# Optimization experiments

Hardware: AMD Instinct MI355X
Metric: run time of the kernel (lower is better)

The kernel has to match this reference:

```python
import jax, jax.numpy as jnp
import numpy as np

N, E, D, G, L = 100000, 1600000, 32, 64, 3
BN_EPS = 1e-5


def setup_inputs() -> dict:
    key = jax.random.key(0)
    ks = jax.random.split(key, 8)
    x = jax.random.normal(ks[0], (N, D), dtype=jnp.float32)
    edge_index = jax.random.randint(ks[1], (2, E), 0, N, dtype=jnp.int64)
    batch = jnp.sort(jax.random.randint(ks[2], (N,), 0, G, dtype=jnp.int64))
    layer_weights = jnp.ones((L,), dtype=jnp.float32)
    # linears[i]: Linear(D->D) + BN(D) (inference-mode stats) ; L of them
    lin_W = jax.random.normal(ks[3], (L, D, D), dtype=jnp.float32) * (1.0 / np.sqrt(D))
    lin_b = jnp.zeros((L, D), dtype=jnp.float32)
    lin_gamma = jnp.ones((L, D), dtype=jnp.float32)
    lin_beta = jnp.zeros((L, D), dtype=jnp.float32)
    lin_mean = jnp.zeros((L, D), dtype=jnp.float32)
    lin_var = jnp.ones((L, D), dtype=jnp.float32)
    # GINConv MLPs: Linear(D->D) + BN(D) + ELU ; L-1 of them
    conv_W = jax.random.normal(ks[4], (L - 1, D, D), dtype=jnp.float32) * (1.0 / np.sqrt(D))
    conv_b = jnp.zeros((L - 1, D), dtype=jnp.float32)
    conv_gamma = jnp.ones((L - 1, D), dtype=jnp.float32)
    conv_beta = jnp.zeros((L - 1, D), dtype=jnp.float32)
    conv_mean = jnp.zeros((L - 1, D), dtype=jnp.float32)
    conv_var = jnp.ones((L - 1, D), dtype=jnp.float32)
    return {"x": x, "edge_index": edge_index, "batch": batch,
            "layer_weights": layer_weights,
            "lin_W": lin_W, "lin_b": lin_b, "lin_gamma": lin_gamma,
            "lin_beta": lin_beta, "lin_mean": lin_mean, "lin_var": lin_var,
            "conv_W": conv_W, "conv_b": conv_b, "conv_gamma": conv_gamma,
            "conv_beta": conv_beta, "conv_mean": conv_mean, "conv_var": conv_var}


def _mlp(h, W, b, gamma, beta, mean, var):
    # Linear -> BatchNorm1d (inference stats) -> ELU
    h = h @ W + b
    h = (h - mean) * (gamma * jax.lax.rsqrt(var + BN_EPS)) + beta
    return jax.nn.elu(h)


def reference(x, edge_index, batch, layer_weights,
              lin_W, lin_b, lin_gamma, lin_beta, lin_mean, lin_var,
              conv_W, conv_b, conv_gamma, conv_beta, conv_mean, conv_var):
    src, dst = edge_index[0], edge_index[1]
    z = _mlp(x, lin_W[0], lin_b[0], lin_gamma[0], lin_beta[0], lin_mean[0], lin_var[0])
    Z = layer_weights[0] * z
    out = jax.ops.segment_max(z, batch, num_segments=G)  # global_max_pool
    for l in range(1, L):
        # GINConv (eps=0): x' = MLP(x + sum_{j->i} x_j)
        agg = jax.ops.segment_sum(x[src], dst, num_segments=N)
        x = _mlp(x + agg, conv_W[l - 1], conv_b[l - 1], conv_gamma[l - 1],
                 conv_beta[l - 1], conv_mean[l - 1], conv_var[l - 1])
        z = layer_weights[l] * _mlp(x, lin_W[l], lin_b[l], lin_gamma[l],
                                    lin_beta[l], lin_mean[l], lin_var[l])
        Z = Z + z
        out = out + jax.ops.segment_max(z, batch, num_segments=G)
    # dropout p=0.0 is identity
    return (out, Z, x)
```

## Files before the change

kernel.cpp:

```cpp
#include <hip/hip_runtime.h>
#include <math.h>

#define N_NODES 100000
#define N_EDGES 1600000
#define DIM 32
#define N_GROUPS 64
#define BN_EPS 1e-5f

#define BIN_NODES 128
#define NBINS ((N_NODES + BIN_NODES - 1) / BIN_NODES)
#define EPB_HIST 2048
#define HIST_BLOCKS ((N_EDGES + EPB_HIST - 1) / EPB_HIST)
#define EPB_SCAT 8192
#define SCAT_SUB (EPB_SCAT / EPB_HIST)
#define SCAT_BLOCKS ((N_EDGES + EPB_SCAT - 1) / EPB_SCAT)
#define GF2_BLOCKS ((N_NODES + 127) / 128)
#define CNT_PAD 16

#define CS_BPG 16
#define CS_BLOCKS ((NBINS + CS_BPG - 1) / CS_BPG)

#define HLS 40

typedef __attribute__((ext_vector_type(8))) short short8;
typedef __attribute__((ext_vector_type(4))) float f32x4;
typedef __attribute__((ext_vector_type(4))) unsigned u32x4;

__device__ __forceinline__ unsigned enc_f32(float f) {
    unsigned u = __float_as_uint(f);
    return (u & 0x80000000u) ? ~u : (u | 0x80000000u);
}
__device__ __forceinline__ float dec_f32(unsigned u) {
    return (u & 0x80000000u) ? __uint_as_float(u & 0x7FFFFFFFu) : __uint_as_float(~u);
}
__device__ __forceinline__ unsigned short f2bf(float f) {
    unsigned u = __float_as_uint(f);
    u += 0x7FFFu + ((u >> 16) & 1u);
    return (unsigned short)(u >> 16);
}

__global__ __launch_bounds__(256) void foldhist_kernel(
        const float* __restrict__ lin_W, const float* __restrict__ lin_b,
        const float* __restrict__ lin_gamma, const float* __restrict__ lin_beta,
        const float* __restrict__ lin_mean, const float* __restrict__ lin_var,
        const float* __restrict__ conv_W, const float* __restrict__ conv_b,
        const float* __restrict__ conv_gamma, const float* __restrict__ conv_beta,
        const float* __restrict__ conv_mean, const float* __restrict__ conv_var,
        float* __restrict__ shf, unsigned short* __restrict__ Wfb,
        unsigned short* __restrict__ x0b, unsigned short* __restrict__ xbufb,
        const int* __restrict__ dst, int* __restrict__ blockcnt)
{
    __shared__ int cnt[NBINS];
    int bid = blockIdx.x;
    int t = threadIdx.x;
    if (bid >= 6) {
        int hb = bid - 6;
        for (int b = t; b < NBINS; b += 256) cnt[b] = 0;
        __syncthreads();
        int base = hb * EPB_HIST;
        for (int i = 0; i < EPB_HIST / 256; ++i) {
            int e = base + i * 256 + t;
            if (e < N_EDGES) atomicAdd(&cnt[dst[e] >> 7], 1);
        }
        __syncthreads();
        for (int b = t; b < NBINS; b += 256)
            blockcnt[(size_t)hb * NBINS + b] = cnt[b];
        return;
    }
    if (bid == 5) {
        if (t < DIM) {
            x0b[(size_t)N_NODES * DIM + t] = 0;
            xbufb[(size_t)N_NODES * DIM + t] = 0;
        }
        return;
    }
    const float *W, *b, *gm, *bt, *mn, *vr;
    if (bid < 3) {
        W = lin_W + bid * DIM * DIM; b = lin_b + bid * DIM; gm = lin_gamma + bid * DIM;
        bt = lin_beta + bid * DIM;   mn = lin_mean + bid * DIM; vr = lin_var + bid * DIM;
    } else {
        int c = bid - 3;
        W = conv_W + c * DIM * DIM; b = conv_b + c * DIM; gm = conv_gamma + c * DIM;
        bt = conv_beta + c * DIM;   mn = conv_mean + c * DIM; vr = conv_var + c * DIM;
    }
    for (int idx = t; idx < DIM * DIM; idx += 256) {
        int j = idx & (DIM - 1);
        float scale = gm[j] / sqrtf(vr[j] + BN_EPS);
        Wfb[bid * DIM * DIM + idx] = f2bf(W[idx] * scale);
    }
    if (t < DIM) {
        float scale = gm[t] / sqrtf(vr[t] + BN_EPS);
        shf[bid * DIM + t] = (b[t] - mn[t]) * scale + bt[t];
    }
}

__global__ __launch_bounds__(256) void colsum_scan_kernel(
        const int* __restrict__ blockcnt,
        int* __restrict__ bincnt,
        int* __restrict__ binoff, int* __restrict__ bincur,
        int* __restrict__ done)
{
    __shared__ int sums[16][CS_BPG];
    __shared__ int sscan[256];
    __shared__ int tick;
    int t = threadIdx.x;
    int g = blockIdx.x;
    int bl = t & 15;
    int h0 = t >> 4;
    int b = g * CS_BPG + bl;
    int s = 0;
    if (b < NBINS) {
        for (int hb = h0; hb < HIST_BLOCKS; hb += 16)
            s += blockcnt[(size_t)hb * NBINS + b];
    }
    sums[h0][bl] = s;
    __syncthreads();
    if (t < CS_BPG && (g * CS_BPG + t) < NBINS) {
        int tot = 0;
#pragma unroll
        for (int h = 0; h < 16; ++h) tot += sums[h][t];
        atomicExch(&bincnt[(g * CS_BPG + t) * CNT_PAD], tot);
    }
    __threadfence();
    __syncthreads();
    if (t == 0) tick = atomicAdd(done, 1);
    __syncthreads();
    if (tick == (int)gridDim.x - 1) {
        int i0 = t * 4;
        int c0 = (i0 + 0 < NBINS) ? atomicAdd(&bincnt[(i0 + 0) * CNT_PAD], 0) : 0;
        int c1 = (i0 + 1 < NBINS) ? atomicAdd(&bincnt[(i0 + 1) * CNT_PAD], 0) : 0;
        int c2 = (i0 + 2 < NBINS) ? atomicAdd(&bincnt[(i0 + 2) * CNT_PAD], 0) : 0;
        int c3 = (i0 + 3 < NBINS) ? atomicAdd(&bincnt[(i0 + 3) * CNT_PAD], 0) : 0;
        int local = c0 + c1 + c2 + c3;
        sscan[t] = local;
        __syncthreads();
        for (int off = 1; off < 256; off <<= 1) {
            int u = (t >= off) ? sscan[t - off] : 0;
            __syncthreads();
            sscan[t] += u;
            __syncthreads();
        }
        int run = sscan[t] - local;
        if (i0 + 0 < NBINS) { binoff[i0 + 0] = run; bincur[(i0 + 0) * CNT_PAD] = run; run += c0; }
        if (i0 + 1 < NBINS) { binoff[i0 + 1] = run; bincur[(i0 + 1) * CNT_PAD] = run; run += c1; }
        if (i0 + 2 < NBINS) { binoff[i0 + 2] = run; bincur[(i0 + 2) * CNT_PAD] = run; run += c2; }
        if (i0 + 3 < NBINS) { binoff[i0 + 3] = run; bincur[(i0 + 3) * CNT_PAD] = run; run += c3; }
        if (t == 0) binoff[NBINS] = N_EDGES;
    }
}

__global__ __launch_bounds__(512) void scatter_linz_kernel(
        const int* __restrict__ src, const int* __restrict__ dst,
        int* __restrict__ bincur, unsigned* __restrict__ binbuf,
        const int* __restrict__ blockcnt,
        const float* __restrict__ x0, unsigned short* __restrict__ x0b,
        const unsigned short* __restrict__ Wb, const float* __restrict__ shfv,
        const int* __restrict__ batch, const float* __restrict__ lw_ptr,
        float* __restrict__ Z, unsigned* __restrict__ segmax)
{
    __shared__ int smem[NBINS];
    int t = threadIdx.x;

    if (blockIdx.x < SCAT_BLOCKS) {
        int* pos = smem;
        for (int b = t; b < NBINS; b += 512) {
            int c = 0;
#pragma unroll
            for (int k = 0; k < SCAT_SUB; ++k) {
                int r = blockIdx.x * SCAT_SUB + k;
                if (r < HIST_BLOCKS)
                    c += blockcnt[(size_t)r * NBINS + b];
            }
            pos[b] = (c > 0) ? atomicAdd(&bincur[b * CNT_PAD], c) : 0;
        }
        __syncthreads();
        int base = blockIdx.x * EPB_SCAT;
        for (int i = 0; i < EPB_SCAT / 512; ++i) {
            int e = base + i * 512 + t;
            if (e < N_EDGES) {
                int d = dst[e];
                int bin = d >> 7;
                int p = atomicAdd(&pos[bin], 1);
                binbuf[p] = ((unsigned)(d & 127) << 17) | (unsigned)src[e];
            }
        }
        return;
    }

    unsigned* segloc = (unsigned*)smem;
    if (t < 8 * DIM) segloc[t] = 0;

    int wv = t >> 6, lane = t & 63;
    int m = lane & 15, kg = lane >> 4;

    short8 b0, b1;
#pragma unroll
    for (int j = 0; j < 8; ++j) {
        int k = kg * 8 + j;
        b0[j] = (short)Wb[k * DIM + m];
        b1[j] = (short)Wb[k * DIM + 16 + m];
    }
    float sh0 = shfv[m], sh1 = shfv[m + 16];
    float lw = lw_ptr[0];
    int blk0 = (blockIdx.x - SCAT_BLOCKS) * 128;
    int gfirst = batch[blk0];
    int row0 = blk0 + wv * 16;
    __syncthreads();

    if (row0 < N_NODES) {
        const float* rp = x0 + (size_t)(row0 + m) * DIM + kg * 8;
        f32x4 v0 = *(const f32x4*)rp;
        f32x4 v1 = *(const f32x4*)(rp + 4);
        short8 a;
        a[0] = (short)f2bf(v0[0]); a[1] = (short)f2bf(v0[1]);
        a[2] = (short)f2bf(v0[2]); a[3] = (short)f2bf(v0[3]);
        a[4] = (short)f2bf(v1[0]); a[5] = (short)f2bf(v1[1]);
        a[6] = (short)f2bf(v1[2]); a[7] = (short)f2bf(v1[3]);
        *(short8*)(x0b + (size_t)(row0 + m) * DIM + kg * 8) = a;

        f32x4 d0 = {0.f, 0.f, 0.f, 0.f}, d1 = {0.f, 0.f, 0.f, 0.f};
        d0 = __builtin_amdgcn_mfma_f32_16x16x32_bf16(a, b0, d0, 0, 0, 0);
        d1 = __builtin_amdgcn_mfma_f32_16x16x32_bf16(a, b1, d1, 0, 0, 0);
#pragma unroll
        for (int r = 0; r < 4; ++r) {
            int row = row0 + kg * 4 + r;
            float a0 = d0[r] + sh0;
            float a1 = d1[r] + sh1;
            float z0 = a0 > 0.f ? a0 : expm1f(a0);
            float z1 = a1 > 0.f ? a1 : expm1f(a1);
            size_t zi = (size_t)row * DIM;
            Z[zi + m] = lw * z0;
            Z[zi + 16 + m] = lw * z1;
            int g = batch[row];
            int go = g - gfirst;
            if (go < 8) {
                atomicMax(&segloc[go * DIM + m], enc_f32(z0));
                atomicMax(&segloc[go * DIM + 16 + m], enc_f32(z1));
            } else {
                atomicMax(&segmax[g * DIM + m], enc_f32(z0));
                atomicMax(&segmax[g * DIM + 16 + m], enc_f32(z1));
            }
        }
    }
    __syncthreads();
    if (t < 8 * DIM) {
        unsigned v = segloc[t];
        if (v) atomicMax(&segmax[(gfirst + (t >> 5)) * DIM + (t & 31)], v);
    }
}

__global__ __launch_bounds__(256) void binsort_kernel(const unsigned* __restrict__ binbuf,
                                                      const int* __restrict__ binoff,
                                                      int* __restrict__ esrc,
                                                      int* __restrict__ nodeptr) {
    __shared__ int cnt[BIN_NODES];
    __shared__ int sc[BIN_NODES];
    int t = threadIdx.x;
    int bin = blockIdx.x;
    int beg = binoff[bin], end = binoff[bin + 1];
    if (t < BIN_NODES) cnt[t] = 0;
    __syncthreads();
    for (int e = beg + t; e < end; e += 256)
        atomicAdd(&cnt[binbuf[e] >> 17], 1);
    __syncthreads();
    int v = (t < BIN_NODES) ? cnt[t] : 0;
    if (t < BIN_NODES) sc[t] = v;
    __syncthreads();
    for (int off = 1; off < BIN_NODES; off <<= 1) {
        int u = (t < BIN_NODES && t >= off) ? sc[t - off] : 0;
        __syncthreads();
        if (t < BIN_NODES) sc[t] += u;
        __syncthreads();
    }
    if (t < BIN_NODES) {
        int excl = sc[t] - v;
        cnt[t] = excl;
        nodeptr[bin * BIN_NODES + t] = beg + excl;
    }
    __syncthreads();
    for (int e = beg + t; e < end; e += 256) {
        unsigned pe = binbuf[e];
        int dl = (int)(pe >> 17);
        int p = atomicAdd(&cnt[dl], 1);
        esrc[beg + p] = (int)(pe & 0x1FFFFu);
    }
}

#define GIN_FETCH4(I0, A)                                                       \
  {                                                                             \
    _Pragma("unroll")                                                           \
    for (int q_ = 0; q_ < 4; ++q_) {                                            \
      int ii_ = (I0) + q_;                                                      \
      int ei_ = beg + ii_;                                                      \
      ei_ = ei_ < (N_EDGES - 1) ? ei_ : (N_EDGES - 1);                          \
      int s_ = esrc[ei_];                                                       \
      s_ = (ii_ < deg) ? s_ : N_NODES;                                          \
      A[q_] = *(const short8*)(xb + (size_t)s_ * DIM + kg8);                    \
    }                                                                           \
  }

#define GIN_MFMA4(A)                                                            \
  {                                                                             \
    _Pragma("unroll")                                                           \
    for (int q_ = 0; q_ < 4; ++q_) {                                            \
      d0[q_] = __builtin_amdgcn_mfma_f32_16x16x32_bf16(A[q_], bc0, d0[q_], 0, 0, 0); \
      d1[q_] = __builtin_amdgcn_mfma_f32_16x16x32_bf16(A[q_], bc1, d1[q_], 0, 0, 0); \
    }                                                                           \
  }

__global__ __launch_bounds__(256) void gin_fused_kernel(
        const unsigned short* __restrict__ xb,
        const int* __restrict__ esrc,
        const int* __restrict__ nodeptr,
        const unsigned short* __restrict__ Wcb, const float* __restrict__ shc,
        const unsigned short* __restrict__ Wlb, const float* __restrict__ shl,
        const int* __restrict__ batch, const float* __restrict__ lw_ptr,
        unsigned short* __restrict__ xnextb,
        float* __restrict__ xoutf,
        float* __restrict__ Z,
        unsigned* __restrict__ segmax)
{
    __shared__ __align__(16) unsigned short hl[4][16 * HLS];
    __shared__ unsigned segloc[8 * DIM];
    int t = threadIdx.x;
    segloc[t] = 0;

    int wv = t >> 6, lane = t & 63;
    int m = lane & 15, kg = lane >> 4;
    int kg8 = kg * 8;

    short8 bc0, bc1, bl0, bl1;
#pragma unroll
    for (int j = 0; j < 8; ++j) {
        int k = kg8 + j;
        bc0[j] = (short)Wcb[k * DIM + m];
        bc1[j] = (short)Wcb[k * DIM + 16 + m];
        bl0[j] = (short)Wlb[k * DIM + m];
        bl1[j] = (short)Wlb[k * DIM + 16 + m];
    }
    float shc0 = shc[m], shc1 = shc[m + 16];
    float shl0 = shl[m], shl1 = shl[m + 16];
    float lw = lw_ptr[0];
    int blk0 = blockIdx.x * 64;
    int gfirst = batch[blk0 < N_NODES ? blk0 : N_NODES - 1];
    int row0 = blk0 + wv * 16;
    __syncthreads();

    if (row0 < N_NODES) {
        int beg = nodeptr[row0 + m];
        int deg = nodeptr[row0 + m + 1] - beg;
        int md = deg;
#pragma unroll
        for (int off = 1; off < 16; off <<= 1)
            md = max(md, __shfl_xor(md, off, 64));

        short8 aS = *(const short8*)(xb + (size_t)(row0 + m) * DIM + kg8);
        f32x4 d0[4], d1[4];
#pragma unroll
        for (int q = 0; q < 4; ++q) {
            d0[q] = (f32x4){0.f, 0.f, 0.f, 0.f};
            d1[q] = (f32x4){0.f, 0.f, 0.f, 0.f};
        }
        d0[0] = __builtin_amdgcn_mfma_f32_16x16x32_bf16(aS, bc0, d0[0], 0, 0, 0);
        d1[0] = __builtin_amdgcn_mfma_f32_16x16x32_bf16(aS, bc1, d1[0], 0, 0, 0);

        int B = (md + 3) >> 2;
        if (B > 0) {
            short8 aA[4], aB[4];
            GIN_FETCH4(0, aA);
            int k = 1;
            for (; k + 1 < B; k += 2) {
                GIN_FETCH4(4 * k, aB);
                GIN_MFMA4(aA);
                GIN_FETCH4(4 * (k + 1), aA);
                GIN_MFMA4(aB);
            }
            if (k < B) {
                GIN_FETCH4(4 * k, aB);
                GIN_MFMA4(aA);
                GIN_MFMA4(aB);
            } else {
                GIN_MFMA4(aA);
            }
        }

        float hp0[4], hp1[4];
#pragma unroll
        for (int r = 0; r < 4; ++r) {
            float a0 = d0[0][r] + d0[1][r] + d0[2][r] + d0[3][r] + shc0;
            float a1 = d1[0][r] + d1[1][r] + d1[2][r] + d1[3][r] + shc1;
            hp0[r] = a0 > 0.f ? a0 : expm1f(a0);
            hp1[r] = a1 > 0.f ? a1 : expm1f(a1);
        }
#pragma unroll
        for (int r = 0; r < 4; ++r) {
            hl[wv][(kg * 4 + r) * HLS + m] = f2bf(hp0[r]);
            hl[wv][(kg * 4 + r) * HLS + 16 + m] = f2bf(hp1[r]);
        }
        if (xoutf) {
#pragma unroll
            for (int r = 0; r < 4; ++r) {
                int row = row0 + kg * 4 + r;
                xoutf[(size_t)row * DIM + m] = hp0[r];
                xoutf[(size_t)row * DIM + 16 + m] = hp1[r];
            }
        }
        if (xnextb) {
            int ii = lane >> 2, q = lane & 3;
            u32x4 pk = *(const u32x4*)&hl[wv][ii * HLS + q * 8];
            *(u32x4*)(xnextb + (size_t)(row0 + ii) * DIM + q * 8) = pk;
        }

        short8 a2 = *(const short8*)&hl[wv][m * HLS + kg8];
        f32x4 e0 = {0.f, 0.f, 0.f, 0.f}, e1 = {0.f, 0.f, 0.f, 0.f};
        e0 = __builtin_amdgcn_mfma_f32_16x16x32_bf16(a2, bl0, e0, 0, 0, 0);
        e1 = __builtin_amdgcn_mfma_f32_16x16x32_bf16(a2, bl1, e1, 0, 0, 0);
#pragma unroll
        for (int r = 0; r < 4; ++r) {
            int row = row0 + kg * 4 + r;
            float a0 = e0[r] + shl0, a1 = e1[r] + shl1;
            float z0 = a0 > 0.f ? a0 : expm1f(a0);
            float z1 = a1 > 0.f ? a1 : expm1f(a1);
            float zw0 = lw * z0, zw1 = lw * z1;
            size_t zi = (size_t)row * DIM;
            Z[zi + m] += zw0;
            Z[zi + 16 + m] += zw1;
            int g = batch[row];
            int go = g - gfirst;
            if (go < 8) {
                atomicMax(&segloc[go * DIM + m], enc_f32(zw0));
                atomicMax(&segloc[go * DIM + 16 + m], enc_f32(zw1));
            } else {
                atomicMax(&segmax[g * DIM + m], enc_f32(zw0));
                atomicMax(&segmax[g * DIM + 16 + m], enc_f32(zw1));
            }
        }
    }
    __syncthreads();
    unsigned v = segloc[t];
    if (v) atomicMax(&segmax[(gfirst + (t >> 5)) * DIM + (t & 31)], v);
}

__global__ void add_out3_kernel(const unsigned* __restrict__ s0,
                                const unsigned* __restrict__ s1,
                                const unsigned* __restrict__ s2,
                                float* __restrict__ out) {
    int t = blockIdx.x * blockDim.x + threadIdx.x;
    out[t] = dec_f32(s0[t]) + dec_f32(s1[t]) + dec_f32(s2[t]);
}

extern "C" void kernel_launch(void* const* d_in, const int* in_sizes, int n_in,
                              void* d_out, int out_size, void* d_ws, size_t ws_size,
                              hipStream_t stream) {
    const float* x0        = (const float*)d_in[0];
    const int*   ei        = (const int*)d_in[1];
    const int*   batch     = (const int*)d_in[2];
    const float* lw        = (const float*)d_in[3];
    const float* lin_W     = (const float*)d_in[4];
    const float* lin_b     = (const float*)d_in[5];
    const float* lin_gamma = (const float*)d_in[6];
    const float* lin_beta  = (const float*)d_in[7];
    const float* lin_mean  = (const float*)d_in[8];
    const float* lin_var   = (const float*)d_in[9];
    const float* conv_W    = (const float*)d_in[10];
    const float* conv_b    = (const float*)d_in[11];
    const float* conv_gamma= (const float*)d_in[12];
    const float* conv_beta = (const float*)d_in[13];
    const float* conv_mean = (const float*)d_in[14];
    const float* conv_var  = (const float*)d_in[15];

    float* out  = (float*)d_out;
    float* Z    = out + N_GROUPS * DIM;
    float* xout = Z + (size_t)N_NODES * DIM;

    char* p = (char*)d_ws;
    unsigned short* x0b     = (unsigned short*)p; p += ((size_t)N_NODES * DIM + 8192) * sizeof(unsigned short);
    unsigned short* xbufb   = (unsigned short*)p; p += ((size_t)N_NODES * DIM + 8192) * sizeof(unsigned short);
    unsigned*       binbuf  = (unsigned*)p;       p += (size_t)N_EDGES * sizeof(unsigned);
    int*            esrc    = (int*)p;            p += (size_t)N_EDGES * sizeof(int);
    int*            nodeptr = (int*)p;            p += (NBINS * BIN_NODES + 1) * sizeof(int);
    unsigned*       segmx   = (unsigned*)p;       p += 3 * N_GROUPS * DIM * sizeof(unsigned);
    int*            bincnt  = (int*)p;            p += NBINS * CNT_PAD * sizeof(int);
    int*            donec   = (int*)p;            p += 16 * sizeof(int);
    int*            binoff  = (int*)p;            p += (NBINS + 1) * sizeof(int);
    int*            bincur  = (int*)p;            p += NBINS * CNT_PAD * sizeof(int);
    float*          shf     = (float*)p;          p += 5 * DIM * sizeof(float);
    unsigned short* Wfb     = (unsigned short*)p; p += 5 * DIM * DIM * sizeof(unsigned short);

    int* blockcnt = (int*)xbufb;

    const int* src = ei;
    const int* dst = ei + N_EDGES;

    const int gf_blocks = (N_NODES + 63) / 64;

    (void)hipMemsetAsync(segmx, 0,
                         (3 * N_GROUPS * DIM + NBINS * CNT_PAD + 16) * sizeof(unsigned), stream);

    foldhist_kernel<<<6 + HIST_BLOCKS, 256, 0, stream>>>(
        lin_W, lin_b, lin_gamma, lin_beta, lin_mean, lin_var,
        conv_W, conv_b, conv_gamma, conv_beta, conv_mean, conv_var,
        shf, Wfb, x0b, xbufb, dst, blockcnt);

    colsum_scan_kernel<<<CS_BLOCKS, 256, 0, stream>>>(blockcnt, bincnt,
                                                      binoff, bincur, donec);

    scatter_linz_kernel<<<SCAT_BLOCKS + GF2_BLOCKS, 512, 0, stream>>>(
        src, dst, bincur, binbuf, blockcnt,
        x0, x0b, Wfb, shf, batch, lw, Z, segmx);

    binsort_kernel<<<NBINS, 256, 0, stream>>>(binbuf, binoff, esrc, nodeptr);

    gin_fused_kernel<<<gf_blocks, 256, 0, stream>>>(x0b, esrc, nodeptr,
                                                    Wfb + 3 * DIM * DIM, shf + 3 * DIM,
                                                    Wfb + 1 * DIM * DIM, shf + 1 * DIM,
                                                    batch, lw + 1,
                                                    xbufb, (float*)nullptr, Z,
                                                    segmx + N_GROUPS * DIM);

    gin_fused_kernel<<<gf_blocks, 256, 0, stream>>>(xbufb, esrc, nodeptr,
                                                    Wfb + 4 * DIM * DIM, shf + 4 * DIM,
                                                    Wfb + 2 * DIM * DIM, shf + 2 * DIM,
                                                    batch, lw + 2,
                                                    (unsigned short*)nullptr, xout, Z,
                                                    segmx + 2 * N_GROUPS * DIM);

    add_out3_kernel<<<8, 256, 0, stream>>>(segmx, segmx + N_GROUPS * DIM,
                                           segmx + 2 * N_GROUPS * DIM, out);
}
```

Before: 229.3 us.

## Fuse bin sort into first GIN layer and final output sum into second

The per-bin edge sort now runs inside the first GIN kernel. Each 512-thread block sorts one 128-node bin and then processes those same nodes using the begin and degree values it kept in shared memory. The separate add_out3 kernel is folded into the second GIN kernel through a last-block-done counter that sums the three segment-max buffers. This removes two kernel launches and the round trip of nodeptr through global memory, but the first layer now serialises the sort and GIN phases within each block, and the block size doubles.

```diff
diff --git a/kernel.cpp b/kernel.cpp
--- a/kernel.cpp
+++ b/kernel.cpp
@@ -14,7 +14,6 @@
 #define EPB_SCAT 8192
 #define SCAT_SUB (EPB_SCAT / EPB_HIST)
 #define SCAT_BLOCKS ((N_EDGES + EPB_SCAT - 1) / EPB_SCAT)
-#define GF2_BLOCKS ((N_NODES + 127) / 128)
 #define CNT_PAD 16
 
 #define CS_BPG 16
@@ -249,43 +248,6 @@
     }
 }
 
-__global__ __launch_bounds__(256) void binsort_kernel(const unsigned* __restrict__ binbuf,
-                                                      const int* __restrict__ binoff,
-                                                      int* __restrict__ esrc,
-                                                      int* __restrict__ nodeptr) {
-    __shared__ int cnt[BIN_NODES];
-    __shared__ int sc[BIN_NODES];
-    int t = threadIdx.x;
-    int bin = blockIdx.x;
-    int beg = binoff[bin], end = binoff[bin + 1];
-    if (t < BIN_NODES) cnt[t] = 0;
-    __syncthreads();
-    for (int e = beg + t; e < end; e += 256)
-        atomicAdd(&cnt[binbuf[e] >> 17], 1);
-    __syncthreads();
-    int v = (t < BIN_NODES) ? cnt[t] : 0;
-    if (t < BIN_NODES) sc[t] = v;
-    __syncthreads();
-    for (int off = 1; off < BIN_NODES; off <<= 1) {
-        int u = (t < BIN_NODES && t >= off) ? sc[t - off] : 0;
-        __syncthreads();
-        if (t < BIN_NODES) sc[t] += u;
-        __syncthreads();
-    }
-    if (t < BIN_NODES) {
-        int excl = sc[t] - v;
-        cnt[t] = excl;
-        nodeptr[bin * BIN_NODES + t] = beg + excl;
-    }
-    __syncthreads();
-    for (int e = beg + t; e < end; e += 256) {
-        unsigned pe = binbuf[e];
-        int dl = (int)(pe >> 17);
-        int p = atomicAdd(&cnt[dl], 1);
-        esrc[beg + p] = (int)(pe & 0x1FFFFu);
-    }
-}
-
 #define GIN_FETCH4(I0, A)                                                       \
   {                                                                             \
     _Pragma("unroll")                                                           \
@@ -308,22 +270,67 @@
     }                                                                           \
   }
 
-__global__ __launch_bounds__(256) void gin_fused_kernel(
+__global__ __launch_bounds__(512) void gin_fused_kernel(
         const unsigned short* __restrict__ xb,
-        const int* __restrict__ esrc,
-        const int* __restrict__ nodeptr,
+        const unsigned* __restrict__ binbuf,
+        const int* __restrict__ binoff,
+        int* __restrict__ esrc,
+        int* __restrict__ nodeptr,
+        int do_sort,
         const unsigned short* __restrict__ Wcb, const float* __restrict__ shc,
         const unsigned short* __restrict__ Wlb, const float* __restrict__ shl,
         const int* __restrict__ batch, const float* __restrict__ lw_ptr,
         unsigned short* __restrict__ xnextb,
         float* __restrict__ xoutf,
         float* __restrict__ Z,
-        unsigned* __restrict__ segmax)
+        unsigned* __restrict__ segmax,
+        unsigned* __restrict__ sm0, unsigned* __restrict__ sm1,
+        float* __restrict__ outv, int* __restrict__ done)
 {
-    __shared__ __align__(16) unsigned short hl[4][16 * HLS];
+    __shared__ __align__(16) unsigned short hl[8][16 * HLS];
     __shared__ unsigned segloc[8 * DIM];
+    __shared__ int cnt[BIN_NODES];
+    __shared__ int sc[BIN_NODES];
+    __shared__ int begL[BIN_NODES];
+    __shared__ int degL[BIN_NODES];
+    __shared__ int lastt;
     int t = threadIdx.x;
-    segloc[t] = 0;
+    if (t < 8 * DIM) segloc[t] = 0;
+
+    int bin = blockIdx.x;
+
+    if (do_sort) {
+        int sbeg = binoff[bin], send = binoff[bin + 1];
+        if (t < BIN_NODES) cnt[t] = 0;
+        __syncthreads();
+        for (int e = sbeg + t; e < send; e += 512)
+            atomicAdd(&cnt[binbuf[e] >> 17], 1);
+        __syncthreads();
+        int v = (t < BIN_NODES) ? cnt[t] : 0;
+        if (t < BIN_NODES) sc[t] = v;
+        __syncthreads();
+        for (int off = 1; off < BIN_NODES; off <<= 1) {
+            int u = (t < BIN_NODES && t >= off) ? sc[t - off] : 0;
+            __syncthreads();
+            if (t < BIN_NODES) sc[t] += u;
+            __syncthreads();
+        }
+        if (t < BIN_NODES) {
+            int excl = sc[t] - v;
+            cnt[t] = excl;
+            begL[t] = sbeg + excl;
+            degL[t] = v;
+            nodeptr[bin * BIN_NODES + t] = sbeg + excl;
+        }
+        __syncthreads();
+        for (int e = sbeg + t; e < send; e += 512) {
+            unsigned pe = binbuf[e];
+            int dl = (int)(pe >> 17);
+            int p = atomicAdd(&cnt[dl], 1);
+            esrc[sbeg + p] = (int)(pe & 0x1FFFFu);
+        }
+    }
+    __syncthreads();
 
     int wv = t >> 6, lane = t & 63;
     int m = lane & 15, kg = lane >> 4;
@@ -341,14 +348,20 @@
     float shc0 = shc[m], shc1 = shc[m + 16];
     float shl0 = shl[m], shl1 = shl[m + 16];
     float lw = lw_ptr[0];
-    int blk0 = blockIdx.x * 64;
-    int gfirst = batch[blk0 < N_NODES ? blk0 : N_NODES - 1];
+    int blk0 = bin * BIN_NODES;
+    int gfirst = batch[blk0];
     int row0 = blk0 + wv * 16;
-    __syncthreads();
 
     if (row0 < N_NODES) {
-        int beg = nodeptr[row0 + m];
-        int deg = nodeptr[row0 + m + 1] - beg;
+        int li = wv * 16 + m;
+        int beg, deg;
+        if (do_sort) {
+            beg = begL[li];
+            deg = degL[li];
+        } else {
+            beg = nodeptr[row0 + m];
+            deg = nodeptr[row0 + m + 1] - beg;
+        }
         int md = deg;
 #pragma unroll
         for (int off = 1; off < 16; off <<= 1)
@@ -437,16 +450,25 @@
         }
     }
     __syncthreads();
-    unsigned v = segloc[t];
-    if (v) atomicMax(&segmax[(gfirst + (t >> 5)) * DIM + (t & 31)], v);
-}
-
-__global__ void add_out3_kernel(const unsigned* __restrict__ s0,
-                                const unsigned* __restrict__ s1,
-                                const unsigned* __restrict__ s2,
-                                float* __restrict__ out) {
-    int t = blockIdx.x * blockDim.x + threadIdx.x;
-    out[t] = dec_f32(s0[t]) + dec_f32(s1[t]) + dec_f32(s2[t]);
+    if (t < 8 * DIM) {
+        unsigned v = segloc[t];
+        if (v) atomicMax(&segmax[(gfirst + (t >> 5)) * DIM + (t & 31)], v);
+    }
+
+    if (outv) {
+        __threadfence();
+        __syncthreads();
+        if (t == 0) lastt = atomicAdd(done, 1);
+        __syncthreads();
+        if (lastt == (int)gridDim.x - 1) {
+            for (int i = t; i < N_GROUPS * DIM; i += 512) {
+                unsigned a = atomicAdd(&sm0[i], 0u);
+                unsigned b = atomicAdd(&sm1[i], 0u);
+                unsigned c = atomicAdd(&segmax[i], 0u);
+                outv[i] = dec_f32(a) + dec_f32(b) + dec_f32(c);
+            }
+        }
+    }
 }
 
 extern "C" void kernel_launch(void* const* d_in, const int* in_sizes, int n_in,
@@ -492,8 +514,6 @@
     const int* src = ei;
     const int* dst = ei + N_EDGES;
 
-    const int gf_blocks = (N_NODES + 63) / 64;
-
     (void)hipMemsetAsync(segmx, 0,
                          (3 * N_GROUPS * DIM + NBINS * CNT_PAD + 16) * sizeof(unsigned), stream);
 
@@ -505,26 +525,25 @@
     colsum_scan_kernel<<<CS_BLOCKS, 256, 0, stream>>>(blockcnt, bincnt,
                                                       binoff, bincur, donec);
 
-    scatter_linz_kernel<<<SCAT_BLOCKS + GF2_BLOCKS, 512, 0, stream>>>(
+    scatter_linz_kernel<<<SCAT_BLOCKS + NBINS, 512, 0, stream>>>(
         src, dst, bincur, binbuf, blockcnt,
         x0, x0b, Wfb, shf, batch, lw, Z, segmx);
 
-    binsort_kernel<<<NBINS, 256, 0, stream>>>(binbuf, binoff, esrc, nodeptr);
-
-    gin_fused_kernel<<<gf_blocks, 256, 0, stream>>>(x0b, esrc, nodeptr,
-                                                    Wfb + 3 * DIM * DIM, shf + 3 * DIM,
-                                                    Wfb + 1 * DIM * DIM, shf + 1 * DIM,
-                                                    batch, lw + 1,
-                                                    xbufb, (float*)nullptr, Z,
-                                                    segmx + N_GROUPS * DIM);
-
-    gin_fused_kernel<<<gf_blocks, 256, 0, stream>>>(xbufb, esrc, nodeptr,
-                                                    Wfb + 4 * DIM * DIM, shf + 4 * DIM,
-                                                    Wfb + 2 * DIM * DIM, shf + 2 * DIM,
-                                                    batch, lw + 2,
-                                                    (unsigned short*)nullptr, xout, Z,
-                                                    segmx + 2 * N_GROUPS * DIM);
-
-    add_out3_kernel<<<8, 256, 0, stream>>>(segmx, segmx + N_GROUPS * DIM,
-                                           segmx + 2 * N_GROUPS * DIM, out);
-}
+    gin_fused_kernel<<<NBINS, 512, 0, stream>>>(x0b, binbuf, binoff, esrc, nodeptr, 1,
+                                                Wfb + 3 * DIM * DIM, shf + 3 * DIM,
+                                                Wfb + 1 * DIM * DIM, shf + 1 * DIM,
+                                                batch, lw + 1,
+                                                xbufb, (float*)nullptr, Z,
+                                                segmx + N_GROUPS * DIM,
+                                                (unsigned*)nullptr, (unsigned*)nullptr,
+                                                (float*)nullptr, (int*)nullptr);
+
+    gin_fused_kernel<<<NBINS, 512, 0, stream>>>(xbufb, binbuf, binoff, esrc, nodeptr, 0,
+                                                Wfb + 4 * DIM * DIM, shf + 4 * DIM,
+                                                Wfb + 2 * DIM * DIM, shf + 2 * DIM,
+                                                batch, lw + 2,
+                                                (unsigned short*)nullptr, xout, Z,
+                                                segmx + 2 * N_GROUPS * DIM,
+                                                segmx, segmx + N_GROUPS * DIM,
+                                                out, donec + 1);
+}
```

Result: slower. 386.0 us (+68.3%).
